# Kernel tuning notes

Hardware: AMD Instinct MI355X
Metric: run time of the kernel (lower is better)

## Reference

```python
import jax, jax.numpy as jnp
import numpy as np

B, N, DIN, DE, NH, DK = 4, 256, 128, 64, 8, 16


def setup_inputs() -> dict:
    key = jax.random.key(0)
    ks = jax.random.split(key, 8)
    s = 0.05
    return {
        "h": jax.random.normal(ks[0], (B, N, DIN), jnp.float32),
        "e": jax.random.normal(ks[1], (B, N, N, DE), jnp.float32),
        "mask": jnp.ones((B, N), jnp.float32),
        "WQ": jax.random.normal(ks[2], (DIN, NH * DK), jnp.float32) * s,
        "WK": jax.random.normal(ks[3], (DIN, NH * DK), jnp.float32) * s,
        "WV": jax.random.normal(ks[4], (DIN, NH * DK), jnp.float32) * s,
        "WE": jax.random.normal(ks[5], (DE, NH * DK), jnp.float32) * s,
        "WE2": jax.random.normal(ks[6], (DE, NH * DK), jnp.float32) * s,
    }


def reference(h, e, mask, WQ, WK, WV, WE, WE2):
    b, n, _ = h.shape
    Q = (h @ WQ).reshape(b, n, NH, DK)
    K = (h @ WK).reshape(b, n, NH, DK) * (float(DK) ** -0.5)
    V = (h @ WV).reshape(b, n, NH, DK)
    E = (e @ WE).reshape(b, n, n, NH, DK)
    E2 = (e @ WE2).reshape(b, n, n, NH, DK)
    # edge-augmented scores: (b, i, j, h, k)
    scores = jnp.einsum('bihk,bjhk->bijh', Q, K)[..., None] + E2
    scores = jnp.exp(jnp.clip(scores, -5.0, 5.0))
    attn_mask = mask[:, :, None, None, None] * mask[:, None, :, None, None]
    scores = scores * attn_mask
    softmax_denom = jnp.clip(scores.sum(axis=2), 1e-6, None)  # (b,i,h,k)
    scores = scores * attn_mask  # attn_dropout p=0.0 -> identity
    out = jnp.einsum('bijhk,bjhk->bihk', scores, V)
    out = out + (scores * E).sum(axis=2)
    out = out / softmax_denom
    return out.reshape(b, n, NH * DK)
```

## Files before the change

kernel.cpp:

```cpp
#include <hip/hip_runtime.h>

#define BB   4
#define NN   256
#define DIN  128
#define DE   64
#define NH   8
#define DK   16
#define CC   128

typedef __attribute__((ext_vector_type(8))) short short8;
typedef __attribute__((ext_vector_type(4))) float f32x4;

__device__ __forceinline__ unsigned short f2bfu(float f) {
    union { float f; unsigned int i; } v; v.f = f;
    unsigned int x = v.i;
    x += 0x7FFFu + ((x >> 16) & 1u);
    return (unsigned short)(x >> 16);
}

__global__ __launch_bounds__(256) void wprep_kernel(
    const float* __restrict__ WE, const float* __restrict__ WE2,
    unsigned short* __restrict__ wfrag)
{
    const int tid  = blockIdx.x * 256 + threadIdx.x;
    const int m    = tid >> 10;
    const int g    = (tid >> 7) & 7;
    const int ks   = (tid >> 6) & 1;
    const int lane = tid & 63;
    const int q4 = lane >> 4, l15 = lane & 15;
    const float* W = m ? WE2 : WE;
    union { uint4 u; unsigned short s[8]; } pk;
    #pragma unroll
    for (int ii = 0; ii < 8; ++ii) {
        const int d = ks * 32 + q4 * 8 + ii;
        pk.s[ii] = f2bfu(W[d * CC + g * 16 + l15]);
    }
    ((uint4*)wfrag)[tid] = pk.u;
}

__global__ __launch_bounds__(256) void qkv_kernel(
    const float* __restrict__ h, const float* __restrict__ WQ,
    const float* __restrict__ WK, const float* __restrict__ WV,
    float* __restrict__ Qw, float* __restrict__ Kw, float* __restrict__ Vw)
{
    __shared__ float hsh[4 * DIN];
    __shared__ float psum[4 * 1536];
    const int t  = threadIdx.x;
    const int r0 = blockIdx.x * 4;

    hsh[t]       = h[(size_t)r0 * DIN + t];
    hsh[256 + t] = h[(size_t)r0 * DIN + 256 + t];
    __syncthreads();

    const int cp  = t & 63;
    const int qtr = t >> 6;
    float aq[4][2], ak[4][2], av[4][2];
    #pragma unroll
    for (int r = 0; r < 4; ++r) {
        aq[r][0]=aq[r][1]=ak[r][0]=ak[r][1]=av[r][0]=av[r][1]=0.f;
    }
    #pragma unroll 4
    for (int dd = 0; dd < 32; ++dd) {
        const int d = qtr * 32 + dd;
        const float2 fq = ((const float2*)WQ)[d * 64 + cp];
        const float2 fk = ((const float2*)WK)[d * 64 + cp];
        const float2 fv = ((const float2*)WV)[d * 64 + cp];
        #pragma unroll
        for (int r = 0; r < 4; ++r) {
            const float hd = hsh[r * DIN + d];
            aq[r][0] = fmaf(hd, fq.x, aq[r][0]); aq[r][1] = fmaf(hd, fq.y, aq[r][1]);
            ak[r][0] = fmaf(hd, fk.x, ak[r][0]); ak[r][1] = fmaf(hd, fk.y, ak[r][1]);
            av[r][0] = fmaf(hd, fv.x, av[r][0]); av[r][1] = fmaf(hd, fv.y, av[r][1]);
        }
    }
    float* pq = psum + qtr * 1536;
    #pragma unroll
    for (int r = 0; r < 4; ++r) {
        pq[r*384       + 2*cp] = aq[r][0]; pq[r*384       + 2*cp+1] = aq[r][1];
        pq[r*384 + 128 + 2*cp] = ak[r][0]; pq[r*384 + 128 + 2*cp+1] = ak[r][1];
        pq[r*384 + 256 + 2*cp] = av[r][0]; pq[r*384 + 256 + 2*cp+1] = av[r][1];
    }
    __syncthreads();
    #pragma unroll
    for (int k = 0; k < 6; ++k) {
        const int o = k * 256 + t;
        float v = psum[o] + psum[1536 + o] + psum[3072 + o] + psum[4608 + o];
        const int r   = o / 384;
        const int mc  = o - r * 384;
        const int mat = mc >> 7;
        const int c   = mc & 127;
        const size_t idx = (size_t)(r0 + r) * CC + c;
        if      (mat == 0) Qw[idx] = v;
        else if (mat == 1) Kw[idx] = v * 0.25f;
        else               Vw[idx] = v;
    }
}

__global__ __launch_bounds__(256, 3) void attn_kernel(
    const float* __restrict__ e, const float* __restrict__ maskp,
    const unsigned short* __restrict__ wfrag,
    const float* __restrict__ Qw, const float* __restrict__ Kw,
    const float* __restrict__ Vw, float* __restrict__ out)
{
    __shared__ __align__(16) unsigned short esh[NN * DE];
    __shared__ float qk_sh[NN * 9];
    __shared__ float msk_sh[NN];
    __shared__ float qrow_sh[CC];

    const int row  = blockIdx.x;
    const int b    = row >> 8, i = row & 255;
    const int t    = threadIdx.x;
    const int wave = t >> 6, lane = t & 63;
    const int q4   = lane >> 4;
    const int l15  = lane & 15;

    {
        const float4* src = (const float4*)(e + (size_t)row * NN * DE);
        uint4* dst = (uint4*)esh;
        #pragma unroll
        for (int r = 0; r < 8; ++r) {
            const int cidx = r * 256 + t;
            const int j = cidx >> 3, ch = cidx & 7;
            const float4 f0 = src[2 * cidx];
            const float4 f1 = src[2 * cidx + 1];
            union { uint4 u; unsigned short s[8]; } pk;
            pk.s[0]=f2bfu(f0.x); pk.s[1]=f2bfu(f0.y); pk.s[2]=f2bfu(f0.z); pk.s[3]=f2bfu(f0.w);
            pk.s[4]=f2bfu(f1.x); pk.s[5]=f2bfu(f1.y); pk.s[6]=f2bfu(f1.z); pk.s[7]=f2bfu(f1.w);
            dst[j * 8 + (ch ^ (j & 7))] = pk.u;
        }
    }
    if (t < CC) qrow_sh[t] = Qw[(size_t)row * CC + t];
    msk_sh[t] = maskp[b * NN + t];

    short8 bfrag[2][2][2];
    {
        const uint4* wf = (const uint4*)wfrag;
        #pragma unroll
        for (int m = 0; m < 2; ++m)
        #pragma unroll
        for (int ct = 0; ct < 2; ++ct) {
            const int g = wave * 2 + ct;
            #pragma unroll
            for (int ks = 0; ks < 2; ++ks) {
                union { uint4 u; short8 s8; } cv;
                cv.u = wf[((m * 8 + g) * 2 + ks) * 64 + lane];
                bfrag[m][ct][ks] = cv.s8;
            }
        }
    }
    __syncthreads();

    {
        const float4* kr = (const float4*)(Kw + (size_t)(b * NN + t) * CC);
        #pragma unroll
        for (int hh = 0; hh < NH; ++hh) {
            float s = 0.f;
            #pragma unroll
            for (int p = 0; p < 4; ++p) {
                const float4 kv = kr[hh * 4 + p];
                const int qb = hh * 16 + p * 4;
                s += kv.x * qrow_sh[qb]     + kv.y * qrow_sh[qb + 1]
                   + kv.z * qrow_sh[qb + 2] + kv.w * qrow_sh[qb + 3];
            }
            qk_sh[t * 9 + hh] = s;
        }
    }
    __syncthreads();

    const float mi = msk_sh[i];
    float acc[2] = {0.f, 0.f}, dnm[2] = {0.f, 0.f};
    const short8* ep = (const short8*)esh;

    #pragma unroll 2
    for (int s = 0; s < 16; ++s) {
        const int ja = s * 16 + l15;
        const short8 a0 = ep[ja * 8 + ((q4    ) ^ (ja & 7))];
        const short8 a1 = ep[ja * 8 + ((q4 + 4) ^ (ja & 7))];
        #pragma unroll
        for (int ct = 0; ct < 2; ++ct) {
            const int g = wave * 2 + ct;
            f32x4 s2 = {0.f,0.f,0.f,0.f}, eE = {0.f,0.f,0.f,0.f};
            s2 = __builtin_amdgcn_mfma_f32_16x16x32_bf16(a0, bfrag[1][ct][0], s2, 0,0,0);
            s2 = __builtin_amdgcn_mfma_f32_16x16x32_bf16(a1, bfrag[1][ct][1], s2, 0,0,0);
            eE = __builtin_amdgcn_mfma_f32_16x16x32_bf16(a0, bfrag[0][ct][0], eE, 0,0,0);
            eE = __builtin_amdgcn_mfma_f32_16x16x32_bf16(a1, bfrag[0][ct][1], eE, 0,0,0);
            const float* vrow = Vw + (size_t)(b*NN + s*16 + q4*4) * CC + g*16 + l15;
            #pragma unroll
            for (int r = 0; r < 4; ++r) {
                const int jr = s * 16 + q4 * 4 + r;
                float sc = qk_sh[jr * 9 + g] + s2[r];
                sc = fminf(5.f, fmaxf(-5.f, sc));
                const float p  = __expf(sc);
                const float mm = mi * msk_sh[jr];
                const float s1 = p * mm;
                dnm[ct] += s1;
                const float vv = vrow[r * CC];
                acc[ct] = fmaf(s1 * mm, vv + eE[r], acc[ct]);
            }
        }
    }

    #pragma unroll
    for (int ct = 0; ct < 2; ++ct) {
        float a = acc[ct], d = dnm[ct];
        a += __shfl_xor(a, 16); a += __shfl_xor(a, 32);
        d += __shfl_xor(d, 16); d += __shfl_xor(d, 32);
        acc[ct] = a; dnm[ct] = d;
    }
    if (lane < 32) {
        const int ct = lane >> 4;
        out[(size_t)row * CC + wave * 32 + lane] = acc[ct] / fmaxf(dnm[ct], 1e-6f);
    }
}

extern "C" void kernel_launch(void* const* d_in, const int* in_sizes, int n_in,
                              void* d_out, int out_size, void* d_ws, size_t ws_size,
                              hipStream_t stream)
{
    const float* h    = (const float*)d_in[0];
    const float* e    = (const float*)d_in[1];
    const float* mask = (const float*)d_in[2];
    const float* WQ   = (const float*)d_in[3];
    const float* WK   = (const float*)d_in[4];
    const float* WV   = (const float*)d_in[5];
    const float* WE   = (const float*)d_in[6];
    const float* WE2  = (const float*)d_in[7];

    unsigned short* wfrag = (unsigned short*)d_ws;
    float* Qw = (float*)((char*)d_ws + 32768);
    float* Kw = Qw + BB * NN * CC;
    float* Vw = Kw + BB * NN * CC;

    wprep_kernel<<<8,   256, 0, stream>>>(WE, WE2, wfrag);
    qkv_kernel <<<256,  256, 0, stream>>>(h, WQ, WK, WV, Qw, Kw, Vw);
    attn_kernel<<<BB*NN, 256, 0, stream>>>(e, mask, wfrag, Qw, Kw, Vw,
                                           (float*)d_out);
}
```

Before: 139.2 us.

## Halve edge LDS tile, transpose V, merge weight prep into QKV kernel

The attention kernel now stages the edge row in two halves of 128 neighbours instead of all 256, which cuts its LDS footprint so the launch bound can go from 3 to 6 blocks per CU. V is written transposed (feature-major), so each lane fetches four consecutive neighbour values with one float4 load. The qk scratch is laid out head-major. The separate bf16 weight-fragment prep kernel is folded into extra blocks of the QKV kernel, saving one launch. The cost is an extra pair of barriers per block and less load/compute overlap within a block, since the second half is loaded only after the first is consumed.

```diff
diff --git a/kernel.cpp b/kernel.cpp
--- a/kernel.cpp
+++ b/kernel.cpp
@@ -18,34 +18,35 @@
     return (unsigned short)(x >> 16);
 }
 
-__global__ __launch_bounds__(256) void wprep_kernel(
-    const float* __restrict__ WE, const float* __restrict__ WE2,
-    unsigned short* __restrict__ wfrag)
-{
-    const int tid  = blockIdx.x * 256 + threadIdx.x;
-    const int m    = tid >> 10;
-    const int g    = (tid >> 7) & 7;
-    const int ks   = (tid >> 6) & 1;
-    const int lane = tid & 63;
-    const int q4 = lane >> 4, l15 = lane & 15;
-    const float* W = m ? WE2 : WE;
-    union { uint4 u; unsigned short s[8]; } pk;
-    #pragma unroll
-    for (int ii = 0; ii < 8; ++ii) {
-        const int d = ks * 32 + q4 * 8 + ii;
-        pk.s[ii] = f2bfu(W[d * CC + g * 16 + l15]);
-    }
-    ((uint4*)wfrag)[tid] = pk.u;
-}
-
 __global__ __launch_bounds__(256) void qkv_kernel(
     const float* __restrict__ h, const float* __restrict__ WQ,
     const float* __restrict__ WK, const float* __restrict__ WV,
-    float* __restrict__ Qw, float* __restrict__ Kw, float* __restrict__ Vw)
+    const float* __restrict__ WE, const float* __restrict__ WE2,
+    float* __restrict__ Qw, float* __restrict__ Kw, float* __restrict__ Vt,
+    unsigned short* __restrict__ wfrag)
 {
+    const int t = threadIdx.x;
+
+    if (blockIdx.x >= 256) {
+        const int tid  = (blockIdx.x - 256) * 256 + t;
+        const int m    = tid >> 10;
+        const int g    = (tid >> 7) & 7;
+        const int ks   = (tid >> 6) & 1;
+        const int lane = tid & 63;
+        const int q4 = lane >> 4, l15 = lane & 15;
+        const float* W = m ? WE2 : WE;
+        union { uint4 u; unsigned short s[8]; } pk;
+        #pragma unroll
+        for (int ii = 0; ii < 8; ++ii) {
+            const int d = ks * 32 + q4 * 8 + ii;
+            pk.s[ii] = f2bfu(W[d * CC + g * 16 + l15]);
+        }
+        ((uint4*)wfrag)[tid] = pk.u;
+        return;
+    }
+
     __shared__ float hsh[4 * DIN];
     __shared__ float psum[4 * 1536];
-    const int t  = threadIdx.x;
     const int r0 = blockIdx.x * 4;
 
     hsh[t]       = h[(size_t)r0 * DIN + t];
@@ -56,9 +57,9 @@
     const int qtr = t >> 6;
     float aq[4][2], ak[4][2], av[4][2];
     #pragma unroll
-    for (int r = 0; r < 4; ++r) {
+    for (int r = 0; r < 4; ++r)
         aq[r][0]=aq[r][1]=ak[r][0]=ak[r][1]=av[r][0]=av[r][1]=0.f;
-    }
+
     #pragma unroll 4
     for (int dd = 0; dd < 32; ++dd) {
         const int d = qtr * 32 + dd;
@@ -81,6 +82,9 @@
         pq[r*384 + 256 + 2*cp] = av[r][0]; pq[r*384 + 256 + 2*cp+1] = av[r][1];
     }
     __syncthreads();
+
+    const int b  = r0 >> 8;
+    const int j0 = r0 & 255;
     #pragma unroll
     for (int k = 0; k < 6; ++k) {
         const int o = k * 256 + t;
@@ -89,21 +93,20 @@
         const int mc  = o - r * 384;
         const int mat = mc >> 7;
         const int c   = mc & 127;
-        const size_t idx = (size_t)(r0 + r) * CC + c;
-        if      (mat == 0) Qw[idx] = v;
-        else if (mat == 1) Kw[idx] = v * 0.25f;
-        else               Vw[idx] = v;
-    }
-}
-
-__global__ __launch_bounds__(256, 3) void attn_kernel(
+        if      (mat == 0) Qw[(size_t)(r0 + r) * CC + c] = v;
+        else if (mat == 1) Kw[(size_t)(r0 + r) * CC + c] = v * 0.25f;
+        else               Vt[((size_t)(b * CC) + c) * NN + j0 + r] = v;
+    }
+}
+
+__global__ __launch_bounds__(256, 6) void attn_kernel(
     const float* __restrict__ e, const float* __restrict__ maskp,
     const unsigned short* __restrict__ wfrag,
     const float* __restrict__ Qw, const float* __restrict__ Kw,
-    const float* __restrict__ Vw, float* __restrict__ out)
+    const float* __restrict__ Vt, float* __restrict__ out)
 {
-    __shared__ __align__(16) unsigned short esh[NN * DE];
-    __shared__ float qk_sh[NN * 9];
+    __shared__ __align__(16) unsigned short esh[128 * DE];
+    __shared__ float qk_sh[NH * NN];
     __shared__ float msk_sh[NN];
     __shared__ float qrow_sh[CC];
 
@@ -114,23 +117,8 @@
     const int q4   = lane >> 4;
     const int l15  = lane & 15;
 
-    {
-        const float4* src = (const float4*)(e + (size_t)row * NN * DE);
-        uint4* dst = (uint4*)esh;
-        #pragma unroll
-        for (int r = 0; r < 8; ++r) {
-            const int cidx = r * 256 + t;
-            const int j = cidx >> 3, ch = cidx & 7;
-            const float4 f0 = src[2 * cidx];
-            const float4 f1 = src[2 * cidx + 1];
-            union { uint4 u; unsigned short s[8]; } pk;
-            pk.s[0]=f2bfu(f0.x); pk.s[1]=f2bfu(f0.y); pk.s[2]=f2bfu(f0.z); pk.s[3]=f2bfu(f0.w);
-            pk.s[4]=f2bfu(f1.x); pk.s[5]=f2bfu(f1.y); pk.s[6]=f2bfu(f1.z); pk.s[7]=f2bfu(f1.w);
-            dst[j * 8 + (ch ^ (j & 7))] = pk.u;
-        }
-    }
-    if (t < CC) qrow_sh[t] = Qw[(size_t)row * CC + t];
-    msk_sh[t] = maskp[b * NN + t];
+    const float4* esrc = (const float4*)(e + (size_t)row * NN * DE);
+    uint4* edst = (uint4*)esh;
 
     short8 bfrag[2][2][2];
     {
@@ -147,6 +135,21 @@
                 bfrag[m][ct][ks] = cv.s8;
             }
         }
+    }
+
+    if (t < CC) qrow_sh[t] = Qw[(size_t)row * CC + t];
+    msk_sh[t] = maskp[b * NN + t];
+
+    #pragma unroll
+    for (int r = 0; r < 4; ++r) {
+        const int cidx = r * 256 + t;
+        const int j = cidx >> 3, ch = cidx & 7;
+        const float4 f0 = esrc[2 * cidx];
+        const float4 f1 = esrc[2 * cidx + 1];
+        union { uint4 u; unsigned short s[8]; } pk;
+        pk.s[0]=f2bfu(f0.x); pk.s[1]=f2bfu(f0.y); pk.s[2]=f2bfu(f0.z); pk.s[3]=f2bfu(f0.w);
+        pk.s[4]=f2bfu(f1.x); pk.s[5]=f2bfu(f1.y); pk.s[6]=f2bfu(f1.z); pk.s[7]=f2bfu(f1.w);
+        edst[j * 8 + (ch ^ (j & 7))] = pk.u;
     }
     __syncthreads();
 
@@ -162,7 +165,7 @@
                 s += kv.x * qrow_sh[qb]     + kv.y * qrow_sh[qb + 1]
                    + kv.z * qrow_sh[qb + 2] + kv.w * qrow_sh[qb + 3];
             }
-            qk_sh[t * 9 + hh] = s;
+            qk_sh[hh * 256 + t] = s;
         }
     }
     __syncthreads();
@@ -171,31 +174,51 @@
     float acc[2] = {0.f, 0.f}, dnm[2] = {0.f, 0.f};
     const short8* ep = (const short8*)esh;
 
-    #pragma unroll 2
-    for (int s = 0; s < 16; ++s) {
-        const int ja = s * 16 + l15;
-        const short8 a0 = ep[ja * 8 + ((q4    ) ^ (ja & 7))];
-        const short8 a1 = ep[ja * 8 + ((q4 + 4) ^ (ja & 7))];
-        #pragma unroll
-        for (int ct = 0; ct < 2; ++ct) {
-            const int g = wave * 2 + ct;
-            f32x4 s2 = {0.f,0.f,0.f,0.f}, eE = {0.f,0.f,0.f,0.f};
-            s2 = __builtin_amdgcn_mfma_f32_16x16x32_bf16(a0, bfrag[1][ct][0], s2, 0,0,0);
-            s2 = __builtin_amdgcn_mfma_f32_16x16x32_bf16(a1, bfrag[1][ct][1], s2, 0,0,0);
-            eE = __builtin_amdgcn_mfma_f32_16x16x32_bf16(a0, bfrag[0][ct][0], eE, 0,0,0);
-            eE = __builtin_amdgcn_mfma_f32_16x16x32_bf16(a1, bfrag[0][ct][1], eE, 0,0,0);
-            const float* vrow = Vw + (size_t)(b*NN + s*16 + q4*4) * CC + g*16 + l15;
+    #pragma unroll
+    for (int hf = 0; hf < 2; ++hf) {
+        if (hf == 1) {
+            __syncthreads();
             #pragma unroll
             for (int r = 0; r < 4; ++r) {
-                const int jr = s * 16 + q4 * 4 + r;
-                float sc = qk_sh[jr * 9 + g] + s2[r];
-                sc = fminf(5.f, fmaxf(-5.f, sc));
-                const float p  = __expf(sc);
-                const float mm = mi * msk_sh[jr];
-                const float s1 = p * mm;
-                dnm[ct] += s1;
-                const float vv = vrow[r * CC];
-                acc[ct] = fmaf(s1 * mm, vv + eE[r], acc[ct]);
+                const int cidx = r * 256 + t;
+                const int j = cidx >> 3, ch = cidx & 7;
+                const float4 f0 = esrc[2048 + 2 * cidx];
+                const float4 f1 = esrc[2048 + 2 * cidx + 1];
+                union { uint4 u; unsigned short s[8]; } pk;
+                pk.s[0]=f2bfu(f0.x); pk.s[1]=f2bfu(f0.y); pk.s[2]=f2bfu(f0.z); pk.s[3]=f2bfu(f0.w);
+                pk.s[4]=f2bfu(f1.x); pk.s[5]=f2bfu(f1.y); pk.s[6]=f2bfu(f1.z); pk.s[7]=f2bfu(f1.w);
+                edst[j * 8 + (ch ^ (j & 7))] = pk.u;
+            }
+            __syncthreads();
+        }
+        #pragma unroll 2
+        for (int s = 0; s < 8; ++s) {
+            const int ja = s * 16 + l15;
+            const short8 a0 = ep[ja * 8 + ((q4    ) ^ (ja & 7))];
+            const short8 a1 = ep[ja * 8 + ((q4 + 4) ^ (ja & 7))];
+            #pragma unroll
+            for (int ct = 0; ct < 2; ++ct) {
+                const int g = wave * 2 + ct;
+                f32x4 s2 = {0.f,0.f,0.f,0.f}, eE = {0.f,0.f,0.f,0.f};
+                s2 = __builtin_amdgcn_mfma_f32_16x16x32_bf16(a0, bfrag[1][ct][0], s2, 0,0,0);
+                s2 = __builtin_amdgcn_mfma_f32_16x16x32_bf16(a1, bfrag[1][ct][1], s2, 0,0,0);
+                eE = __builtin_amdgcn_mfma_f32_16x16x32_bf16(a0, bfrag[0][ct][0], eE, 0,0,0);
+                eE = __builtin_amdgcn_mfma_f32_16x16x32_bf16(a1, bfrag[0][ct][1], eE, 0,0,0);
+                const int j0 = hf * 128 + s * 16 + q4 * 4;
+                const float4 v4 = *(const float4*)
+                    (Vt + ((size_t)(b * CC) + g * 16 + l15) * NN + j0);
+                #pragma unroll
+                for (int r = 0; r < 4; ++r) {
+                    const int jr = j0 + r;
+                    float sc = qk_sh[g * 256 + jr] + s2[r];
+                    sc = fminf(5.f, fmaxf(-5.f, sc));
+                    const float p  = __expf(sc);
+                    const float mm = mi * msk_sh[jr];
+                    const float s1 = p * mm;
+                    dnm[ct] += s1;
+                    const float vv = (r==0)?v4.x:(r==1)?v4.y:(r==2)?v4.z:v4.w;
+                    acc[ct] = fmaf(s1 * mm, vv + eE[r], acc[ct]);
+                }
             }
         }
     }
@@ -229,10 +252,10 @@
     unsigned short* wfrag = (unsigned short*)d_ws;
     float* Qw = (float*)((char*)d_ws + 32768);
     float* Kw = Qw + BB * NN * CC;
-    float* Vw = Kw + BB * NN * CC;
-
-    wprep_kernel<<<8,   256, 0, stream>>>(WE, WE2, wfrag);
-    qkv_kernel <<<256,  256, 0, stream>>>(h, WQ, WK, WV, Qw, Kw, Vw);
-    attn_kernel<<<BB*NN, 256, 0, stream>>>(e, mask, wfrag, Qw, Kw, Vw,
+    float* Vt = Kw + BB * NN * CC;
+
+    qkv_kernel <<<264,   256, 0, stream>>>(h, WQ, WK, WV, WE, WE2,
+                                           Qw, Kw, Vt, wfrag);
+    attn_kernel<<<BB*NN, 256, 0, stream>>>(e, mask, wfrag, Qw, Kw, Vt,
                                            (float*)d_out);
 }
```

Result: slower. 189.9 us (+36.4%).
